# Performance work log

Measured on AMD Instinct MI355X. Metric: run time of the kernel, lower is better.

Reference implementation:

```python
import jax, jax.numpy as jnp
import numpy as np

B, H, P, L = 8, 512, 512, 2048
HIGH_STAB, LOW_STAB = 0.9, 0.99  # 0 <= high < |lambda| <= low <= 1 (discrete dynamics)


def setup_inputs() -> dict:
    key = jax.random.key(0)
    k_u, k_mag, k_ph, k_b, k_c, k_d = jax.random.split(key, 6)
    u = jax.random.normal(k_u, (B, H, L), dtype=jnp.float32)
    # Frozen diagonal reservoir state matrix Lambda_bar: complex eigenvalues with
    # magnitude in (high_stability, low_stability], random phase (stored as real/imag pairs).
    mag = jax.random.uniform(k_mag, (P,), minval=HIGH_STAB, maxval=LOW_STAB)
    phase = jax.random.uniform(k_ph, (P,), minval=0.0, maxval=2.0 * np.pi)
    Lambda_bar_ri = jnp.stack([mag * jnp.cos(phase), mag * jnp.sin(phase)], axis=-1)  # (P,2)
    B_bar_ri = jax.random.normal(k_b, (P, H, 2), dtype=jnp.float32)  # complex B_bar as real pairs
    C_ri = jax.random.normal(k_c, (H, P, 2), dtype=jnp.float32)      # complex C as real pairs
    D = jax.random.normal(k_d, (H, H), dtype=jnp.float32)
    return {"u": u, "Lambda_bar_ri": Lambda_bar_ri, "B_bar_ri": B_bar_ri, "C_ri": C_ri, "D": D}


def _binary_op(e_i, e_j):
    A_i, Bu_i = e_i
    A_j, Bu_j = e_j
    return (A_j * A_i, A_j * Bu_i + Bu_j)


def reference(u, Lambda_bar_ri, B_bar_ri, C_ri, D):
    Lam = jax.lax.complex(Lambda_bar_ri[:, 0], Lambda_bar_ri[:, 1])        # (P,)
    B_bar = jax.lax.complex(B_bar_ri[..., 0], B_bar_ri[..., 1])            # (P,H)
    C = jax.lax.complex(C_ri[..., 0], C_ri[..., 1])                        # (H,P)
    # Bu_t = B_bar @ u_t for all t, batched: (B,P,L) complex
    Bu = jnp.einsum('ph,bhl->bpl', B_bar, u.astype(B_bar.dtype))
    A = jnp.broadcast_to(Lam[None, :, None], Bu.shape)                     # (B,P,L)
    # Parallel associative scan: x_t = Lam * x_{t-1} + Bu_t
    _, x = jax.lax.associative_scan(_binary_op, (A, Bu), axis=2)           # (B,P,L)
    C_A_Bu = jnp.einsum('hp,bpl->bhl', C, x).real                          # (B,H,L)
    # torch.einsum('hh,bhl->bhl', D, u) uses only the diagonal of D
    Du = jnp.diagonal(D)[None, :, None] * u
    return jax.nn.gelu(C_A_Bu + Du, approximate=False)
```

## Files before the change

kernel.cpp:

```cpp
#include <hip/hip_runtime.h>
#include <cstdint>
#include <cstddef>

#define BB 8
#define HH 512
#define PP 512
#define LL 2048

typedef __attribute__((ext_vector_type(8))) __bf16 bf16x8;
typedef __attribute__((ext_vector_type(4))) float f32x4;

__device__ __forceinline__ uint16_t f2bf(float f) {
  uint32_t u = __builtin_bit_cast(uint32_t, f);
  u += 0x7FFFu + ((u >> 16) & 1u);
  return (uint16_t)(u >> 16);
}

__device__ __forceinline__ void async_copy16(const void* gptr, void* ldsptr) {
  __builtin_amdgcn_global_load_lds(
      (const __attribute__((address_space(1))) unsigned int*)gptr,
      (__attribute__((address_space(3))) unsigned int*)ldsptr,
      16, 0, 0);
}

__global__ __launch_bounds__(256) void prep_and_transpose(
    const float* __restrict__ U, const float* __restrict__ Bbar,
    const float* __restrict__ Cri, const float* __restrict__ Dm,
    uint16_t* __restrict__ Ut, uint16_t* __restrict__ A1,
    uint16_t* __restrict__ A2, float* __restrict__ Dd) {
  __shared__ uint16_t tile[64][66];
  const int t = threadIdx.x;
  if (blockIdx.x < 2048) {
    const int bid = blockIdx.x;
    const int b = bid >> 8;
    const int h0 = ((bid >> 5) & 7) * 64;
    const int l0 = (bid & 31) * 64;
    const int r = t >> 2, c = t & 3;
    const float* src = U + ((size_t)(b * 512 + h0 + r)) * 2048 + l0 + c * 16;
#pragma unroll
    for (int q = 0; q < 4; ++q) {
      float4 v = *(const float4*)(src + q * 4);
      *(uint32_t*)&tile[r][c * 16 + q * 4]     = (uint32_t)f2bf(v.x) | ((uint32_t)f2bf(v.y) << 16);
      *(uint32_t*)&tile[r][c * 16 + q * 4 + 2] = (uint32_t)f2bf(v.z) | ((uint32_t)f2bf(v.w) << 16);
    }
    __syncthreads();
    uint16_t* dst = Ut + ((size_t)(b * 2048 + l0 + r)) * 512 + h0 + c * 16;
    uint32_t o[8];
#pragma unroll
    for (int k = 0; k < 8; ++k)
      o[k] = (uint32_t)tile[c * 16 + 2 * k][r] | ((uint32_t)tile[c * 16 + 2 * k + 1][r] << 16);
    *(uint4*)(dst)     = make_uint4(o[0], o[1], o[2], o[3]);
    *(uint4*)(dst + 8) = make_uint4(o[4], o[5], o[6], o[7]);
  } else {
    int idx = (blockIdx.x - 2048) * 256 + t;
    int p = idx >> 9, h = idx & 511;
    A1[(size_t)p * 512 + h]          = f2bf(Bbar[((size_t)p * 512 + h) * 2 + 0]);
    A1[(size_t)(512 + p) * 512 + h]  = f2bf(Bbar[((size_t)p * 512 + h) * 2 + 1]);
    int h2 = idx >> 9, p2 = idx & 511;
    A2[(size_t)h2 * 1024 + p2]        = f2bf( Cri[((size_t)h2 * 512 + p2) * 2 + 0]);
    A2[(size_t)h2 * 1024 + 512 + p2]  = f2bf(-Cri[((size_t)h2 * 512 + p2) * 2 + 1]);
    if (idx < 512) Dd[idx] = Dm[(size_t)idx * 512 + idx];
  }
}

__global__ __launch_bounds__(256) void scan_kernel(
    const float* __restrict__ Lam, uint16_t* __restrict__ Bu) {
  const int gt = blockIdx.x * 256 + threadIdx.x;
  const int wave = gt >> 6, lane = gt & 63;
  const int b = wave >> 9, p = wave & 511;
  const float lr = Lam[p * 2 + 0], li = Lam[p * 2 + 1];
  float ar = lr, ai = li;
#pragma unroll
  for (int s = 0; s < 5; ++s) { float nr = ar * ar - ai * ai, ni = 2.f * ar * ai; ar = nr; ai = ni; }

  uint16_t* rowre = Bu + ((size_t)(b * 1024 + p)) * 2048 + lane * 32;
  uint16_t* rowim = Bu + ((size_t)(b * 1024 + 512 + p)) * 2048 + lane * 32;
  uint4 vr[4], vi[4];
#pragma unroll
  for (int q = 0; q < 4; ++q) { vr[q] = ((const uint4*)rowre)[q]; vi[q] = ((const uint4*)rowim)[q]; }

  float xr[32], xi[32];
  float sr = 0.f, si = 0.f;
#pragma unroll
  for (int q = 0; q < 4; ++q) {
    uint32_t wr[4] = {vr[q].x, vr[q].y, vr[q].z, vr[q].w};
    uint32_t wi[4] = {vi[q].x, vi[q].y, vi[q].z, vi[q].w};
#pragma unroll
    for (int d = 0; d < 4; ++d) {
      float br0 = __builtin_bit_cast(float, wr[d] << 16);
      float bi0 = __builtin_bit_cast(float, wi[d] << 16);
      float br1 = __builtin_bit_cast(float, wr[d] & 0xFFFF0000u);
      float bi1 = __builtin_bit_cast(float, wi[d] & 0xFFFF0000u);
      int j = q * 8 + d * 2;
      float nr = lr * sr - li * si + br0, ni = lr * si + li * sr + bi0;
      sr = nr; si = ni; xr[j] = sr; xi[j] = si;
      nr = lr * sr - li * si + br1; ni = lr * si + li * sr + bi1;
      sr = nr; si = ni; xr[j + 1] = sr; xi[j + 1] = si;
    }
  }
  float Ar = ar, Ai = ai, Sr = sr, Si = si;
#pragma unroll
  for (int off = 1; off < 64; off <<= 1) {
    float pAr = __shfl_up(Ar, off), pAi = __shfl_up(Ai, off);
    float pSr = __shfl_up(Sr, off), pSi = __shfl_up(Si, off);
    if (lane >= off) {
      float tSr = Ar * pSr - Ai * pSi + Sr;
      float tSi = Ar * pSi + Ai * pSr + Si;
      float tAr = Ar * pAr - Ai * pAi;
      float tAi = Ar * pAi + Ai * pAr;
      Sr = tSr; Si = tSi; Ar = tAr; Ai = tAi;
    }
  }
  float Cr = __shfl_up(Sr, 1), Ci = __shfl_up(Si, 1);
  if (lane == 0) { Cr = 0.f; Ci = 0.f; }
  float fr_ = lr * Cr - li * Ci, fi_ = lr * Ci + li * Cr;
#pragma unroll
  for (int j = 0; j < 32; ++j) {
    xr[j] += fr_; xi[j] += fi_;
    float nfr = fr_ * lr - fi_ * li, nfi = fr_ * li + fi_ * lr;
    fr_ = nfr; fi_ = nfi;
  }
#pragma unroll
  for (int q = 0; q < 4; ++q) {
    uint32_t wr[4], wi[4];
#pragma unroll
    for (int d = 0; d < 4; ++d) {
      int j = q * 8 + d * 2;
      wr[d] = (uint32_t)f2bf(xr[j]) | ((uint32_t)f2bf(xr[j + 1]) << 16);
      wi[d] = (uint32_t)f2bf(xi[j]) | ((uint32_t)f2bf(xi[j + 1]) << 16);
    }
    ((uint4*)rowre)[q] = make_uint4(wr[0], wr[1], wr[2], wr[3]);
    ((uint4*)rowim)[q] = make_uint4(wi[0], wi[1], wi[2], wi[3]);
  }
}

__global__ __launch_bounds__(256) void transpose_x(
    const uint16_t* __restrict__ X, uint16_t* __restrict__ Xt) {
  __shared__ uint16_t tile[64][66];
  const int t = threadIdx.x;
  const int b = blockIdx.z, p0 = blockIdx.y * 64, l0 = blockIdx.x * 64;
  const int r = t >> 2, c = t & 3;
  const uint16_t* src = X + ((size_t)(b * 1024 + p0 + r)) * 2048 + l0 + c * 16;
  uint4 v0 = *(const uint4*)(src);
  uint4 v1 = *(const uint4*)(src + 8);
  *(uint32_t*)&tile[r][c * 16 + 0]  = v0.x;
  *(uint32_t*)&tile[r][c * 16 + 2]  = v0.y;
  *(uint32_t*)&tile[r][c * 16 + 4]  = v0.z;
  *(uint32_t*)&tile[r][c * 16 + 6]  = v0.w;
  *(uint32_t*)&tile[r][c * 16 + 8]  = v1.x;
  *(uint32_t*)&tile[r][c * 16 + 10] = v1.y;
  *(uint32_t*)&tile[r][c * 16 + 12] = v1.z;
  *(uint32_t*)&tile[r][c * 16 + 14] = v1.w;
  __syncthreads();
  uint16_t* dst = Xt + ((size_t)(b * 2048 + l0 + r)) * 1024 + p0 + c * 16;
  uint32_t o[8];
#pragma unroll
  for (int k = 0; k < 8; ++k)
    o[k] = (uint32_t)tile[c * 16 + 2 * k][r] | ((uint32_t)tile[c * 16 + 2 * k + 1][r] << 16);
  *(uint4*)(dst)     = make_uint4(o[0], o[1], o[2], o[3]);
  *(uint4*)(dst + 8) = make_uint4(o[4], o[5], o[6], o[7]);
}


#define MFMA_ALL16()                                                          \
  acc[0][0] = __builtin_amdgcn_mfma_f32_16x16x32_bf16(a0, b0v, acc[0][0], 0, 0, 0); \
  acc[0][1] = __builtin_amdgcn_mfma_f32_16x16x32_bf16(a0, b1v, acc[0][1], 0, 0, 0); \
  acc[0][2] = __builtin_amdgcn_mfma_f32_16x16x32_bf16(a0, b2v, acc[0][2], 0, 0, 0); \
  acc[0][3] = __builtin_amdgcn_mfma_f32_16x16x32_bf16(a0, b3v, acc[0][3], 0, 0, 0); \
  acc[1][0] = __builtin_amdgcn_mfma_f32_16x16x32_bf16(a1, b0v, acc[1][0], 0, 0, 0); \
  acc[1][1] = __builtin_amdgcn_mfma_f32_16x16x32_bf16(a1, b1v, acc[1][1], 0, 0, 0); \
  acc[1][2] = __builtin_amdgcn_mfma_f32_16x16x32_bf16(a1, b2v, acc[1][2], 0, 0, 0); \
  acc[1][3] = __builtin_amdgcn_mfma_f32_16x16x32_bf16(a1, b3v, acc[1][3], 0, 0, 0); \
  acc[2][0] = __builtin_amdgcn_mfma_f32_16x16x32_bf16(a2, b0v, acc[2][0], 0, 0, 0); \
  acc[2][1] = __builtin_amdgcn_mfma_f32_16x16x32_bf16(a2, b1v, acc[2][1], 0, 0, 0); \
  acc[2][2] = __builtin_amdgcn_mfma_f32_16x16x32_bf16(a2, b2v, acc[2][2], 0, 0, 0); \
  acc[2][3] = __builtin_amdgcn_mfma_f32_16x16x32_bf16(a2, b3v, acc[2][3], 0, 0, 0); \
  acc[3][0] = __builtin_amdgcn_mfma_f32_16x16x32_bf16(a3, b0v, acc[3][0], 0, 0, 0); \
  acc[3][1] = __builtin_amdgcn_mfma_f32_16x16x32_bf16(a3, b1v, acc[3][1], 0, 0, 0); \
  acc[3][2] = __builtin_amdgcn_mfma_f32_16x16x32_bf16(a3, b2v, acc[3][2], 0, 0, 0); \
  acc[3][3] = __builtin_amdgcn_mfma_f32_16x16x32_bf16(a3, b3v, acc[3][3], 0, 0, 0);

#define GEMM_CORE(KDIM)                                                       \
  constexpr int K = (KDIM), NT = K / 64;                                      \
  __shared__ __align__(16) uint16_t Alds[3][128 * 64];                        \
  __shared__ __align__(16) uint16_t Blds[3][256 * 64];                        \
  const int t = threadIdx.x, lane = t & 63, w = t >> 6;                       \
  const int m0 = blockIdx.y * 128, n0 = blockIdx.x * 256, b = blockIdx.z;     \
                \
  const int rA0 = t >> 3, cA0 = (t & 7) ^ (rA0 & 7);                          \
  const int gA1 = t + 512, rA1 = gA1 >> 3, cA1 = (gA1 & 7) ^ (rA1 & 7);       \
  const uint16_t* pA0 = Amat + (size_t)(m0 + rA0) * K + cA0 * 8;              \
  const uint16_t* pA1 = Amat + (size_t)(m0 + rA1) * K + cA1 * 8;              \
  const int dA0 = t * 8, dA1 = gA1 * 8;                                       \
  const int rB0 = t >> 3, cB0 = (t & 7) ^ (rB0 & 7);                          \
  const int gB1 = t + 512, rB1 = gB1 >> 3, cB1 = (gB1 & 7) ^ (rB1 & 7);       \
  const int gB2 = t + 1024, rB2 = gB2 >> 3, cB2 = (gB2 & 7) ^ (rB2 & 7);      \
  const int gB3 = t + 1536, rB3 = gB3 >> 3, cB3 = (gB3 & 7) ^ (rB3 & 7);      \
  const uint16_t* pB0 = Bt + ((size_t)b * 2048 + n0 + rB0) * K + cB0 * 8;     \
  const uint16_t* pB1 = Bt + ((size_t)b * 2048 + n0 + rB1) * K + cB1 * 8;     \
  const uint16_t* pB2 = Bt + ((size_t)b * 2048 + n0 + rB2) * K + cB2 * 8;     \
  const uint16_t* pB3 = Bt + ((size_t)b * 2048 + n0 + rB3) * K + cB3 * 8;     \
  const int dB0 = t * 8, dB1 = gB1 * 8, dB2 = gB2 * 8, dB3 = gB3 * 8;         \
  const int wm = (w >> 2) * 64, wn = (w & 3) * 64;                            \
  const int fr = lane & 15, fq = lane >> 4;                                   \
  int offA[4], offB[4];                                                       \
  _Pragma("unroll")                                                           \
  for (int i = 0; i < 4; ++i) {                                               \
    int rm = wm + i * 16 + fr;                                                \
    offA[i] = rm * 64 + ((fq ^ (rm & 7)) * 8);                                \
    int rn = wn + i * 16 + fr;                                                \
    offB[i] = rn * 64 + ((fq ^ (rn & 7)) * 8);                                \
  }                                                                           \
  f32x4 acc[4][4];                                                            \
  _Pragma("unroll")                                                           \
  for (int i = 0; i < 4; ++i)                                                 \
    _Pragma("unroll")                                                         \
    for (int j = 0; j < 4; ++j) acc[i][j] = (f32x4){0.f, 0.f, 0.f, 0.f};      \
                                \
  async_copy16(pA0,       &Alds[0][dA0]);                                     \
  async_copy16(pA1,       &Alds[0][dA1]);                                     \
  async_copy16(pB0,       &Blds[0][dB0]);                                     \
  async_copy16(pB1,       &Blds[0][dB1]);                                     \
  async_copy16(pB2,       &Blds[0][dB2]);                                     \
  async_copy16(pB3,       &Blds[0][dB3]);                                     \
  async_copy16(pA0 + 64,  &Alds[1][dA0]);                                     \
  async_copy16(pA1 + 64,  &Alds[1][dA1]);                                     \
  async_copy16(pB0 + 64,  &Blds[1][dB0]);                                     \
  async_copy16(pB1 + 64,  &Blds[1][dB1]);                                     \
  async_copy16(pB2 + 64,  &Blds[1][dB2]);                                     \
  async_copy16(pB3 + 64,  &Blds[1][dB3]);                                     \
  _Pragma("unroll")                                                           \
  for (int kt = 0; kt < NT; ++kt) {                                           \
    const int cur = kt % 3, nb = (kt + 2) % 3;                                \
    if (kt + 1 < NT) asm volatile("s_waitcnt vmcnt(6)" ::: "memory");         \
    else             asm volatile("s_waitcnt vmcnt(0)" ::: "memory");         \
    __builtin_amdgcn_s_barrier();                                             \
    __builtin_amdgcn_sched_barrier(0);                                        \
    const uint16_t* Ab = Alds[cur];                                           \
    const uint16_t* Bb = Blds[cur];                                           \
                                            \
    bf16x8 a0 = *(const bf16x8*)&Ab[offA[0]];                                 \
    bf16x8 a1 = *(const bf16x8*)&Ab[offA[1]];                                 \
    bf16x8 a2 = *(const bf16x8*)&Ab[offA[2]];                                 \
    bf16x8 a3 = *(const bf16x8*)&Ab[offA[3]];                                 \
    bf16x8 b0v = *(const bf16x8*)&Bb[offB[0]];                                \
    bf16x8 b1v = *(const bf16x8*)&Bb[offB[1]];                                \
    bf16x8 b2v = *(const bf16x8*)&Bb[offB[2]];                                \
    bf16x8 b3v = *(const bf16x8*)&Bb[offB[3]];                                \
    if (kt + 2 < NT) {                                                        \
      async_copy16(pA0 + (kt + 2) * 64, &Alds[nb][dA0]);                      \
      async_copy16(pA1 + (kt + 2) * 64, &Alds[nb][dA1]);                      \
      async_copy16(pB0 + (kt + 2) * 64, &Blds[nb][dB0]);                      \
    }                                                                         \
    __builtin_amdgcn_s_barrier();                                             \
    asm volatile("s_waitcnt lgkmcnt(0)" ::: "memory");                        \
    __builtin_amdgcn_s_setprio(1);                                            \
    MFMA_ALL16()                                                              \
    __builtin_amdgcn_s_setprio(0);                                            \
    __builtin_amdgcn_s_barrier();                                             \
                \
    a0 = *(const bf16x8*)&Ab[offA[0] ^ 32];                                   \
    a1 = *(const bf16x8*)&Ab[offA[1] ^ 32];                                   \
    a2 = *(const bf16x8*)&Ab[offA[2] ^ 32];                                   \
    a3 = *(const bf16x8*)&Ab[offA[3] ^ 32];                                   \
    b0v = *(const bf16x8*)&Bb[offB[0] ^ 32];                                  \
    b1v = *(const bf16x8*)&Bb[offB[1] ^ 32];                                  \
    b2v = *(const bf16x8*)&Bb[offB[2] ^ 32];                                  \
    b3v = *(const bf16x8*)&Bb[offB[3] ^ 32];                                  \
    if (kt + 2 < NT) {                                                        \
      async_copy16(pB1 + (kt + 2) * 64, &Blds[nb][dB1]);                      \
      async_copy16(pB2 + (kt + 2) * 64, &Blds[nb][dB2]);                      \
      async_copy16(pB3 + (kt + 2) * 64, &Blds[nb][dB3]);                      \
    }                                                                         \
    __builtin_amdgcn_s_barrier();                                             \
    asm volatile("s_waitcnt lgkmcnt(0)" ::: "memory");                        \
    __builtin_amdgcn_s_setprio(1);                                            \
    MFMA_ALL16()                                                              \
    __builtin_amdgcn_s_setprio(0);                                            \
  }                                                                           \
  asm volatile("s_waitcnt vmcnt(0) lgkmcnt(0)" ::: "memory");

__global__ __launch_bounds__(512) void gemm1_fused(
    const uint16_t* __restrict__ Amat, const uint16_t* __restrict__ Bt,
    uint16_t* __restrict__ Bu) {
  GEMM_CORE(512)
  uint16_t* O = Bu + ((size_t)b * 1024 + m0) * 2048 + n0;
#pragma unroll
  for (int i = 0; i < 4; ++i)
#pragma unroll
    for (int j = 0; j < 4; ++j)
#pragma unroll
      for (int r = 0; r < 4; ++r) {
        int mm = wm + i * 16 + fq * 4 + r;
        int nn = wn + j * 16 + fr;
        O[(size_t)mm * 2048 + nn] = f2bf(acc[i][j][r]);
      }
}

__global__ __launch_bounds__(512) void gemm2_fused(
    const uint16_t* __restrict__ Amat, const uint16_t* __restrict__ Bt,
    float* __restrict__ Out, const float* __restrict__ Dd,
    const float* __restrict__ Uu) {
  GEMM_CORE(1024)
  const size_t base = ((size_t)b * 512 + m0) * 2048 + n0;
  float* O = Out + base;
  const float* Ub = Uu + base;
#pragma unroll
  for (int i = 0; i < 4; ++i)
#pragma unroll
    for (int r = 0; r < 4; ++r) {
      int mm = wm + i * 16 + fq * 4 + r;
      float dv = Dd[m0 + mm];
#pragma unroll
      for (int j = 0; j < 4; ++j) {
        int nn = wn + j * 16 + fr;
        float xv = acc[i][j][r] + dv * Ub[(size_t)mm * 2048 + nn];
        O[(size_t)mm * 2048 + nn] = 0.5f * xv * (1.f + erff(xv * 0.70710678118654752f));
      }
    }
}

extern "C" void kernel_launch(void* const* d_in, const int* in_sizes, int n_in,
                              void* d_out, int out_size, void* d_ws, size_t ws_size,
                              hipStream_t stream) {
  const float* u    = (const float*)d_in[0];
  const float* Lam  = (const float*)d_in[1];
  const float* Bbar = (const float*)d_in[2];
  const float* Cri  = (const float*)d_in[3];
  const float* Dm   = (const float*)d_in[4];
  float* out = (float*)d_out;

  char* ws = (char*)d_ws;
  uint16_t* Bu = (uint16_t*)(ws);
  uint16_t* Xt = (uint16_t*)(ws + 33554432);
  uint16_t* Ut = (uint16_t*)(ws + 33554432);
  uint16_t* A1 = (uint16_t*)(ws + 67108864);
  uint16_t* A2 = (uint16_t*)(ws + 68157440);
  float*    Dd = (float*)   (ws + 69206016);

  prep_and_transpose<<<3072, 256, 0, stream>>>(u, Bbar, Cri, Dm, Ut, A1, A2, Dd);
  gemm1_fused<<<dim3(8, 8, BB), 512, 0, stream>>>(A1, Ut, Bu);
  scan_kernel<<<1024, 256, 0, stream>>>(Lam, Bu);
  transpose_x<<<dim3(32, 16, BB), 256, 0, stream>>>(Bu, Xt);
  gemm2_fused<<<dim3(8, 4, BB), 512, 0, stream>>>(A2, Xt, out, Dd, u);
}
```

Measured before the change: 188.4 us.

## Replace triple-buffered 128x256 GEMM tiles with simpler double-buffered 128x128 tiles

Both GEMMs move from 512-thread blocks computing 128x256 tiles with a hand-scheduled three-stage async LDS pipeline to 256-thread blocks computing 128x128 tiles with a plain double-buffered loop that ends each step in __syncthreads. The grid doubles, raising block count and shrinking LDS per block, which can improve occupancy and tail balance. It drops the explicit vmcnt waits, sched barriers and setprio around the MFMAs, so load/compute overlap depends on the compiler and full barriers. Each B tile is also reused across fewer rows of A.

After: 190.5 us. About the same (+1.2%).

```diff
diff --git a/kernel.cpp b/kernel.cpp
--- a/kernel.cpp
+++ b/kernel.cpp
@@ -161,48 +161,22 @@
   *(uint4*)(dst + 8) = make_uint4(o[4], o[5], o[6], o[7]);
 }
 
-
-#define MFMA_ALL16()                                                          \
-  acc[0][0] = __builtin_amdgcn_mfma_f32_16x16x32_bf16(a0, b0v, acc[0][0], 0, 0, 0); \
-  acc[0][1] = __builtin_amdgcn_mfma_f32_16x16x32_bf16(a0, b1v, acc[0][1], 0, 0, 0); \
-  acc[0][2] = __builtin_amdgcn_mfma_f32_16x16x32_bf16(a0, b2v, acc[0][2], 0, 0, 0); \
-  acc[0][3] = __builtin_amdgcn_mfma_f32_16x16x32_bf16(a0, b3v, acc[0][3], 0, 0, 0); \
-  acc[1][0] = __builtin_amdgcn_mfma_f32_16x16x32_bf16(a1, b0v, acc[1][0], 0, 0, 0); \
-  acc[1][1] = __builtin_amdgcn_mfma_f32_16x16x32_bf16(a1, b1v, acc[1][1], 0, 0, 0); \
-  acc[1][2] = __builtin_amdgcn_mfma_f32_16x16x32_bf16(a1, b2v, acc[1][2], 0, 0, 0); \
-  acc[1][3] = __builtin_amdgcn_mfma_f32_16x16x32_bf16(a1, b3v, acc[1][3], 0, 0, 0); \
-  acc[2][0] = __builtin_amdgcn_mfma_f32_16x16x32_bf16(a2, b0v, acc[2][0], 0, 0, 0); \
-  acc[2][1] = __builtin_amdgcn_mfma_f32_16x16x32_bf16(a2, b1v, acc[2][1], 0, 0, 0); \
-  acc[2][2] = __builtin_amdgcn_mfma_f32_16x16x32_bf16(a2, b2v, acc[2][2], 0, 0, 0); \
-  acc[2][3] = __builtin_amdgcn_mfma_f32_16x16x32_bf16(a2, b3v, acc[2][3], 0, 0, 0); \
-  acc[3][0] = __builtin_amdgcn_mfma_f32_16x16x32_bf16(a3, b0v, acc[3][0], 0, 0, 0); \
-  acc[3][1] = __builtin_amdgcn_mfma_f32_16x16x32_bf16(a3, b1v, acc[3][1], 0, 0, 0); \
-  acc[3][2] = __builtin_amdgcn_mfma_f32_16x16x32_bf16(a3, b2v, acc[3][2], 0, 0, 0); \
-  acc[3][3] = __builtin_amdgcn_mfma_f32_16x16x32_bf16(a3, b3v, acc[3][3], 0, 0, 0);
-
 #define GEMM_CORE(KDIM)                                                       \
   constexpr int K = (KDIM), NT = K / 64;                                      \
-  __shared__ __align__(16) uint16_t Alds[3][128 * 64];                        \
-  __shared__ __align__(16) uint16_t Blds[3][256 * 64];                        \
+  __shared__ __align__(16) uint16_t Alds[2][128 * 64];                        \
+  __shared__ __align__(16) uint16_t Blds[2][128 * 64];                        \
   const int t = threadIdx.x, lane = t & 63, w = t >> 6;                       \
-  const int m0 = blockIdx.y * 128, n0 = blockIdx.x * 256, b = blockIdx.z;     \
-                \
-  const int rA0 = t >> 3, cA0 = (t & 7) ^ (rA0 & 7);                          \
-  const int gA1 = t + 512, rA1 = gA1 >> 3, cA1 = (gA1 & 7) ^ (rA1 & 7);       \
-  const uint16_t* pA0 = Amat + (size_t)(m0 + rA0) * K + cA0 * 8;              \
-  const uint16_t* pA1 = Amat + (size_t)(m0 + rA1) * K + cA1 * 8;              \
-  const int dA0 = t * 8, dA1 = gA1 * 8;                                       \
-  const int rB0 = t >> 3, cB0 = (t & 7) ^ (rB0 & 7);                          \
-  const int gB1 = t + 512, rB1 = gB1 >> 3, cB1 = (gB1 & 7) ^ (rB1 & 7);       \
-  const int gB2 = t + 1024, rB2 = gB2 >> 3, cB2 = (gB2 & 7) ^ (rB2 & 7);      \
-  const int gB3 = t + 1536, rB3 = gB3 >> 3, cB3 = (gB3 & 7) ^ (rB3 & 7);      \
-  const uint16_t* pB0 = Bt + ((size_t)b * 2048 + n0 + rB0) * K + cB0 * 8;     \
-  const uint16_t* pB1 = Bt + ((size_t)b * 2048 + n0 + rB1) * K + cB1 * 8;     \
-  const uint16_t* pB2 = Bt + ((size_t)b * 2048 + n0 + rB2) * K + cB2 * 8;     \
-  const uint16_t* pB3 = Bt + ((size_t)b * 2048 + n0 + rB3) * K + cB3 * 8;     \
-  const int dB0 = t * 8, dB1 = gB1 * 8, dB2 = gB2 * 8, dB3 = gB3 * 8;         \
-  const int wm = (w >> 2) * 64, wn = (w & 3) * 64;                            \
+  const int m0 = blockIdx.y * 128, n0 = blockIdx.x * 128, b = blockIdx.z;     \
+   \
+   \
+  const int r0 = t >> 3;                                                      \
+  const int c0 = (t & 7) ^ (r0 & 7);                                          \
+  const uint16_t* gA0 = Amat + (size_t)(m0 + r0) * K + c0 * 8;                \
+  const uint16_t* gB0 = Bt + ((size_t)b * 2048 + n0 + r0) * K + c0 * 8;       \
+  const int d0 = t * 8;                                                       \
+  const int wm = (w >> 1) * 64, wn = (w & 1) * 64;                            \
   const int fr = lane & 15, fq = lane >> 4;                                   \
+           \
   int offA[4], offB[4];                                                       \
   _Pragma("unroll")                                                           \
   for (int i = 0; i < 4; ++i) {                                               \
@@ -216,71 +190,42 @@
   for (int i = 0; i < 4; ++i)                                                 \
     _Pragma("unroll")                                                         \
     for (int j = 0; j < 4; ++j) acc[i][j] = (f32x4){0.f, 0.f, 0.f, 0.f};      \
-                                \
-  async_copy16(pA0,       &Alds[0][dA0]);                                     \
-  async_copy16(pA1,       &Alds[0][dA1]);                                     \
-  async_copy16(pB0,       &Blds[0][dB0]);                                     \
-  async_copy16(pB1,       &Blds[0][dB1]);                                     \
-  async_copy16(pB2,       &Blds[0][dB2]);                                     \
-  async_copy16(pB3,       &Blds[0][dB3]);                                     \
-  async_copy16(pA0 + 64,  &Alds[1][dA0]);                                     \
-  async_copy16(pA1 + 64,  &Alds[1][dA1]);                                     \
-  async_copy16(pB0 + 64,  &Blds[1][dB0]);                                     \
-  async_copy16(pB1 + 64,  &Blds[1][dB1]);                                     \
-  async_copy16(pB2 + 64,  &Blds[1][dB2]);                                     \
-  async_copy16(pB3 + 64,  &Blds[1][dB3]);                                     \
+                                               \
   _Pragma("unroll")                                                           \
-  for (int kt = 0; kt < NT; ++kt) {                                           \
-    const int cur = kt % 3, nb = (kt + 2) % 3;                                \
-    if (kt + 1 < NT) asm volatile("s_waitcnt vmcnt(6)" ::: "memory");         \
-    else             asm volatile("s_waitcnt vmcnt(0)" ::: "memory");         \
-    __builtin_amdgcn_s_barrier();                                             \
-    __builtin_amdgcn_sched_barrier(0);                                        \
-    const uint16_t* Ab = Alds[cur];                                           \
-    const uint16_t* Bb = Blds[cur];                                           \
-                                            \
-    bf16x8 a0 = *(const bf16x8*)&Ab[offA[0]];                                 \
-    bf16x8 a1 = *(const bf16x8*)&Ab[offA[1]];                                 \
-    bf16x8 a2 = *(const bf16x8*)&Ab[offA[2]];                                 \
-    bf16x8 a3 = *(const bf16x8*)&Ab[offA[3]];                                 \
-    bf16x8 b0v = *(const bf16x8*)&Bb[offB[0]];                                \
-    bf16x8 b1v = *(const bf16x8*)&Bb[offB[1]];                                \
-    bf16x8 b2v = *(const bf16x8*)&Bb[offB[2]];                                \
-    bf16x8 b3v = *(const bf16x8*)&Bb[offB[3]];                                \
-    if (kt + 2 < NT) {                                                        \
-      async_copy16(pA0 + (kt + 2) * 64, &Alds[nb][dA0]);                      \
-      async_copy16(pA1 + (kt + 2) * 64, &Alds[nb][dA1]);                      \
-      async_copy16(pB0 + (kt + 2) * 64, &Blds[nb][dB0]);                      \
+  for (int i = 0; i < 4; ++i) {                                               \
+    async_copy16(gA0 + (size_t)i * 32 * K, &Alds[0][d0 + i * 2048]);          \
+    async_copy16(gB0 + (size_t)i * 32 * K, &Blds[0][d0 + i * 2048]);          \
+  }                                                                           \
+  __syncthreads();                                                            \
+  _Pragma("unroll 2")                                                         \
+  for (int it = 0; it < NT; ++it) {                                           \
+    const int cur = it & 1, nxt = cur ^ 1;                                    \
+    if (it + 1 < NT) {                                                        \
+      const int kb = (it + 1) * 64;                                           \
+      _Pragma("unroll")                                                       \
+      for (int i = 0; i < 4; ++i) {                                           \
+        async_copy16(gA0 + (size_t)i * 32 * K + kb, &Alds[nxt][d0 + i * 2048]); \
+        async_copy16(gB0 + (size_t)i * 32 * K + kb, &Blds[nxt][d0 + i * 2048]); \
+      }                                                                       \
     }                                                                         \
-    __builtin_amdgcn_s_barrier();                                             \
-    asm volatile("s_waitcnt lgkmcnt(0)" ::: "memory");                        \
-    __builtin_amdgcn_s_setprio(1);                                            \
-    MFMA_ALL16()                                                              \
-    __builtin_amdgcn_s_setprio(0);                                            \
-    __builtin_amdgcn_s_barrier();                                             \
-                \
-    a0 = *(const bf16x8*)&Ab[offA[0] ^ 32];                                   \
-    a1 = *(const bf16x8*)&Ab[offA[1] ^ 32];                                   \
-    a2 = *(const bf16x8*)&Ab[offA[2] ^ 32];                                   \
-    a3 = *(const bf16x8*)&Ab[offA[3] ^ 32];                                   \
-    b0v = *(const bf16x8*)&Bb[offB[0] ^ 32];                                  \
-    b1v = *(const bf16x8*)&Bb[offB[1] ^ 32];                                  \
-    b2v = *(const bf16x8*)&Bb[offB[2] ^ 32];                                  \
-    b3v = *(const bf16x8*)&Bb[offB[3] ^ 32];                                  \
-    if (kt + 2 < NT) {                                                        \
-      async_copy16(pB1 + (kt + 2) * 64, &Blds[nb][dB1]);                      \
-      async_copy16(pB2 + (kt + 2) * 64, &Blds[nb][dB2]);                      \
-      async_copy16(pB3 + (kt + 2) * 64, &Blds[nb][dB3]);                      \
+    _Pragma("unroll")                                                         \
+    for (int s = 0; s < 2; ++s) {                                             \
+      const int x = s * 32;                                                   \
+      bf16x8 af[4], bfv[4];                                                   \
+      _Pragma("unroll")                                                       \
+      for (int i = 0; i < 4; ++i) af[i] = *(const bf16x8*)&Alds[cur][offA[i] ^ x]; \
+      _Pragma("unroll")                                                       \
+      for (int j = 0; j < 4; ++j) bfv[j] = *(const bf16x8*)&Blds[cur][offB[j] ^ x]; \
+      _Pragma("unroll")                                                       \
+      for (int i = 0; i < 4; ++i)                                             \
+        _Pragma("unroll")                                                     \
+        for (int j = 0; j < 4; ++j)                                           \
+          acc[i][j] = __builtin_amdgcn_mfma_f32_16x16x32_bf16(af[i], bfv[j], acc[i][j], 0, 0, 0); \
     }                                                                         \
-    __builtin_amdgcn_s_barrier();                                             \
-    asm volatile("s_waitcnt lgkmcnt(0)" ::: "memory");                        \
-    __builtin_amdgcn_s_setprio(1);                                            \
-    MFMA_ALL16()                                                              \
-    __builtin_amdgcn_s_setprio(0);                                            \
-  }                                                                           \
-  asm volatile("s_waitcnt vmcnt(0) lgkmcnt(0)" ::: "memory");
-
-__global__ __launch_bounds__(512) void gemm1_fused(
+    __syncthreads();                                                          \
+  }
+
+__global__ __launch_bounds__(256) void gemm1_fused(
     const uint16_t* __restrict__ Amat, const uint16_t* __restrict__ Bt,
     uint16_t* __restrict__ Bu) {
   GEMM_CORE(512)
@@ -297,7 +242,7 @@
       }
 }
 
-__global__ __launch_bounds__(512) void gemm2_fused(
+__global__ __launch_bounds__(256) void gemm2_fused(
     const uint16_t* __restrict__ Amat, const uint16_t* __restrict__ Bt,
     float* __restrict__ Out, const float* __restrict__ Dd,
     const float* __restrict__ Uu) {
@@ -339,8 +284,8 @@
   float*    Dd = (float*)   (ws + 69206016);
 
   prep_and_transpose<<<3072, 256, 0, stream>>>(u, Bbar, Cri, Dm, Ut, A1, A2, Dd);
-  gemm1_fused<<<dim3(8, 8, BB), 512, 0, stream>>>(A1, Ut, Bu);
+  gemm1_fused<<<dim3(16, 8, BB), 256, 0, stream>>>(A1, Ut, Bu);
   scan_kernel<<<1024, 256, 0, stream>>>(Lam, Bu);
   transpose_x<<<dim3(32, 16, BB), 256, 0, stream>>>(Bu, Xt);
-  gemm2_fused<<<dim3(8, 4, BB), 512, 0, stream>>>(A2, Xt, out, Dd, u);
-}
+  gemm2_fused<<<dim3(16, 4, BB), 256, 0, stream>>>(A2, Xt, out, Dd, u);
+}
```
